# Kernel tuning notes

Hardware: AMD Instinct MI355X
Metric: run time of the kernel (lower is better)

## Reference

```python
import jax, jax.numpy as jnp
import numpy as np

FORWARD_STEPS = 50
DT = 0.01
G = 9.81
BATCH = 131072


def _rot(psi):
    # batched 6x6 block-rotation matrix R(psi)
    b = psi.shape[0]
    c, s = jnp.cos(psi), jnp.sin(psi)
    R = jnp.zeros((b, 6, 6), dtype=psi.dtype)
    R = R.at[:, 0, 0].set(c).at[:, 0, 2].set(-s)
    R = R.at[:, 1, 1].set(c).at[:, 1, 3].set(-s)
    R = R.at[:, 2, 0].set(s).at[:, 2, 2].set(c)
    R = R.at[:, 3, 1].set(s).at[:, 3, 3].set(c)
    R = R.at[:, 4, 4].set(1.0).at[:, 5, 5].set(1.0)
    return R


def setup_inputs() -> dict:
    key = jax.random.key(0)
    k1, k2, k3, k4, k5 = jax.random.split(key, 5)
    b = BATCH
    # build initial full state [b, 1, 8]: keep body-frame Vx away from 0 (A divides by Vx)
    fs = jnp.zeros((b, 8), dtype=jnp.float32)
    fs = fs.at[:, 0].set(jax.random.normal(k1, (b,)) * 0.1)                     # x
    fs = fs.at[:, 1].set(jax.random.uniform(k2, (b,), minval=0.5, maxval=1.5))  # x_dot
    fs = fs.at[:, 2].set(jax.random.normal(k3, (b,)) * 0.1)                     # y
    fs = fs.at[:, 3].set(jax.random.uniform(k4, (b,), minval=-0.2, maxval=0.2)) # y_dot
    fs = fs.at[:, 4].set(jax.random.uniform(k5, (b,), minval=-0.3, maxval=0.3)) # psi
    fs = fs.at[:, 5].set(jax.random.normal(jax.random.fold_in(key, 10), (b,)) * 0.1)  # psi_dot
    fs = fs.at[:, 6].set(jax.random.normal(jax.random.fold_in(key, 11), (b,)) * 0.1)  # accel cmd
    fs = fs.at[:, 7].set(jax.random.uniform(jax.random.fold_in(key, 12), (b,), minval=-0.2, maxval=0.2))  # steer cmd
    full_states = fs[:, None, :]
    actions = jnp.stack([
        jax.random.normal(jax.random.fold_in(key, 20), (b, FORWARD_STEPS)) * 0.1,
        jax.random.uniform(jax.random.fold_in(key, 21), (b, FORWARD_STEPS), minval=-0.2, maxval=0.2),
    ], axis=-1).astype(jnp.float32)
    m = 0.2
    return {
        "full_states": full_states,
        "actions": actions,
        "m": jnp.float32(m),
        "Caf": jnp.float32(5 * 0.25 * m * G),
        "Car": jnp.float32(5 * 0.25 * m * G),
        "lf": jnp.float32(0.05),
        "lr": jnp.float32(0.05),
        "Iz": jnp.float32((0.1 ** 2 + 0.1 ** 2) / 12.0),
    }


def reference(full_states, actions, m, Caf, Car, lf, lr, Iz):
    bsz = full_states.shape[0]
    dt = jnp.asarray(DT, dtype=full_states.dtype)
    state0 = full_states[:, -1, :6]   # [b,6]
    action0 = full_states[:, -1, 6:]  # [b,2]
    acts = jnp.transpose(actions, (1, 0, 2))  # [T,b,2]

    def step(carry, a_next):
        s, u = carry
        psi = s[:, 4]
        Vx = s[:, 1] * jnp.cos(psi) + s[:, 3] * jnp.sin(psi)
        A = jnp.zeros((bsz, 6, 6), dtype=s.dtype)
        A = A.at[:, 0, 1].set(1.0).at[:, 2, 3].set(1.0).at[:, 4, 5].set(1.0)
        A = A.at[:, 3, 3].set(-(2 * Caf + 2 * Car) / (m * Vx))
        A = A.at[:, 3, 5].set(-Vx - (2 * Caf * lf - 2 * Car * lr) / (m * Vx))
        A = A.at[:, 5, 3].set(-(2 * lf * Caf - 2 * lr * Car) / (Iz * Vx))
        A = A.at[:, 5, 4].set(-(2 * lf ** 2 * Caf + 2 * lr ** 2 * Car) / (Iz * Vx))
        Bm = jnp.zeros((bsz, 6, 2), dtype=s.dtype)
        Bm = Bm.at[:, 1, 0].set(1.0)
        Bm = Bm.at[:, 3, 1].set(2 * Caf / m)
        Bm = Bm.at[:, 5, 1].set(2 * lf * Caf / Iz)
        s_body = jnp.einsum('bij,bj->bi', _rot(-psi), s)
        temp = jnp.einsum('bij,bj->bi', A, s_body) + jnp.einsum('bij,bj->bi', Bm, u)
        pred = s + jnp.einsum('bij,bj->bi', _rot(psi), temp) * dt
        out = jnp.concatenate([pred, a_next], axis=1)  # [b,8]
        return (pred, a_next), out

    _, outs = jax.lax.scan(step, (state0, action0), acts)
    return jnp.transpose(outs, (1, 0, 2))  # [b, forward_steps, 8]
```

## Files before the change

### kernel.cpp

```cpp
#include <hip/hip_runtime.h>

#define N_STEPS 50
#define DT 0.01f

__global__ __launch_bounds__(256) void hybrid_sim_kernel(
    const float* __restrict__ fs,
    const float* __restrict__ actions,
    const float* __restrict__ pm,  const float* __restrict__ pCaf,
    const float* __restrict__ pCar, const float* __restrict__ plf,
    const float* __restrict__ plr, const float* __restrict__ pIz,
    float* __restrict__ out, int batch)
{
    int b = blockIdx.x * blockDim.x + threadIdx.x;
    if (b >= batch) return;

    const float4* fsp = (const float4*)(fs + (size_t)b * 8);
    float4 f0 = fsp[0];
    float4 f1 = fsp[1];
    float s0 = f0.x, s1 = f0.y, s2 = f0.z, s3 = f0.w;
    float s4 = f1.x, s5 = f1.y, u0 = f1.z, u1 = f1.w;

    float m  = *pm,  Caf = *pCaf, Car = *pCar;
    float lf = *plf, lr  = *plr,  Iz  = *pIz;
    float k1  = 2.f * (Caf + Car) / m;
    float k2  = 2.f * (Caf * lf - Car * lr) / m;
    float k3  = 2.f * (lf * Caf - lr * Car) / Iz;
    float k4  = 2.f * (lf * lf * Caf + lr * lr * Car) / Iz;
    float b31 = 2.f * Caf / m;
    float b51 = 2.f * lf * Caf / Iz;

    const float4* ap = (const float4*)(actions + (size_t)b * 100);
    float4*       op = (float4*)(out + (size_t)b * 400);

    for (int chunk = 0; chunk < 5; ++chunk) {
        float4 abuf[5];
        #pragma unroll
        for (int j = 0; j < 5; ++j) abuf[j] = ap[chunk * 5 + j];
        const float* av = (const float*)abuf;

        #pragma unroll
        for (int tt = 0; tt < 10; ++tt) {
            float psi = s4;
            float c  = __cosf(psi);
            float sn = __sinf(psi);
            float Vx  = c * s1 + sn * s3;
            float sb3 = c * s3 - sn * s1;
            float inv = __builtin_amdgcn_rcpf(Vx);
            float t3 = -k1 * inv * sb3 + (-Vx - k2 * inv) * s5 + b31 * u1;
            float t5 = -k3 * inv * sb3 - k4 * inv * psi + b51 * u1;
            float p0 = s0 + DT * (c * Vx - sn * sb3);
            float p2 = s2 + DT * (sn * Vx + c * sb3);
            float p1 = s1 + DT * (c * u0 - sn * t3);
            float p3 = s3 + DT * (sn * u0 + c * t3);
            float p4 = s4 + DT * s5;
            float p5 = s5 + DT * t5;

            float nu0 = av[2 * tt];
            float nu1 = av[2 * tt + 1];

            int t = chunk * 10 + tt;
            float4 o0; o0.x = p0; o0.y = p1; o0.z = p2; o0.w = p3;
            float4 o1; o1.x = p4; o1.y = p5; o1.z = nu0; o1.w = nu1;
            op[2 * t]     = o0;
            op[2 * t + 1] = o1;

            s0 = p0; s1 = p1; s2 = p2; s3 = p3; s4 = p4; s5 = p5;
            u0 = nu0; u1 = nu1;
        }
    }
}

extern "C" void kernel_launch(void* const* d_in, const int* in_sizes, int n_in,
                              void* d_out, int out_size, void* d_ws, size_t ws_size,
                              hipStream_t stream) {
    const float* fs      = (const float*)d_in[0];
    const float* actions = (const float*)d_in[1];
    int batch = in_sizes[0] / 8;
    int block = 256;
    int grid  = (batch + block - 1) / block;
    hybrid_sim_kernel<<<grid, block, 0, stream>>>(
        fs, actions,
        (const float*)d_in[2], (const float*)d_in[3], (const float*)d_in[4],
        (const float*)d_in[5], (const float*)d_in[6], (const float*)d_in[7],
        (float*)d_out, batch);
}
```

Measured before the change: 346.9 us.

## Stage per-step outputs in LDS to coalesce global stores

Each thread buffers two timesteps of output (16 floats) in a padded, double-buffered LDS tile. After a block barrier, the wave re-reads the tile transposed so that each 8-lane group writes one element's contiguous 64-byte segment to global memory. This replaces per-lane 32-byte strided stores that touched a different row per lane. It adds LDS traffic and a __syncthreads every two steps, and drops the batch bounds check by assuming the batch is a multiple of 256.

```diff
diff --git a/kernel.cpp b/kernel.cpp
--- a/kernel.cpp
+++ b/kernel.cpp
@@ -1,7 +1,7 @@
 #include <hip/hip_runtime.h>
 
-#define N_STEPS 50
 #define DT 0.01f
+#define ROW 18
 
 __global__ __launch_bounds__(256) void hybrid_sim_kernel(
     const float* __restrict__ fs,
@@ -9,63 +9,86 @@
     const float* __restrict__ pm,  const float* __restrict__ pCaf,
     const float* __restrict__ pCar, const float* __restrict__ plf,
     const float* __restrict__ plr, const float* __restrict__ pIz,
-    float* __restrict__ out, int batch)
+    float* __restrict__ out)
 {
-    int b = blockIdx.x * blockDim.x + threadIdx.x;
-    if (b >= batch) return;
+    __shared__ float lds[2 * 4 * 64 * ROW];
+
+    const int tid  = threadIdx.x;
+    const int lane = tid & 63;
+    const int wv   = tid >> 6;
+    const int b    = blockIdx.x * 256 + tid;
+    const int b0w  = blockIdx.x * 256 + (wv << 6);
 
     const float4* fsp = (const float4*)(fs + (size_t)b * 8);
     float4 f0 = fsp[0];
     float4 f1 = fsp[1];
-    float s0 = f0.x, s1 = f0.y, s2 = f0.z, s3 = f0.w;
-    float s4 = f1.x, s5 = f1.y, u0 = f1.z, u1 = f1.w;
+    float s0=f0.x, s1=f0.y, s2=f0.z, s3=f0.w, s4=f1.x, s5=f1.y, u0=f1.z, u1=f1.w;
 
-    float m  = *pm,  Caf = *pCaf, Car = *pCar;
-    float lf = *plf, lr  = *plr,  Iz  = *pIz;
-    float k1  = 2.f * (Caf + Car) / m;
-    float k2  = 2.f * (Caf * lf - Car * lr) / m;
-    float k3  = 2.f * (lf * Caf - lr * Car) / Iz;
-    float k4  = 2.f * (lf * lf * Caf + lr * lr * Car) / Iz;
-    float b31 = 2.f * Caf / m;
-    float b51 = 2.f * lf * Caf / Iz;
+    float m=*pm, Caf=*pCaf, Car=*pCar, lf=*plf, lr=*plr, Iz=*pIz;
+    float k1  = 2.f*(Caf+Car)/m;
+    float k2  = 2.f*(Caf*lf-Car*lr)/m;
+    float k3  = 2.f*(lf*Caf-lr*Car)/Iz;
+    float k4  = 2.f*(lf*lf*Caf+lr*lr*Car)/Iz;
+    float b31 = 2.f*Caf/m;
+    float b51 = 2.f*lf*Caf/Iz;
 
     const float4* ap = (const float4*)(actions + (size_t)b * 100);
-    float4*       op = (float4*)(out + (size_t)b * 400);
+
+    float* base0 = &lds[(0*4 + wv) * 64 * ROW];
+    float* base1 = &lds[(1*4 + wv) * 64 * ROW];
+
+    float o[16];
 
     for (int chunk = 0; chunk < 5; ++chunk) {
         float4 abuf[5];
         #pragma unroll
-        for (int j = 0; j < 5; ++j) abuf[j] = ap[chunk * 5 + j];
+        for (int j = 0; j < 5; ++j) abuf[j] = ap[chunk*5 + j];
         const float* av = (const float*)abuf;
 
         #pragma unroll
-        for (int tt = 0; tt < 10; ++tt) {
-            float psi = s4;
-            float c  = __cosf(psi);
-            float sn = __sinf(psi);
-            float Vx  = c * s1 + sn * s3;
-            float sb3 = c * s3 - sn * s1;
-            float inv = __builtin_amdgcn_rcpf(Vx);
-            float t3 = -k1 * inv * sb3 + (-Vx - k2 * inv) * s5 + b31 * u1;
-            float t5 = -k3 * inv * sb3 - k4 * inv * psi + b51 * u1;
-            float p0 = s0 + DT * (c * Vx - sn * sb3);
-            float p2 = s2 + DT * (sn * Vx + c * sb3);
-            float p1 = s1 + DT * (c * u0 - sn * t3);
-            float p3 = s3 + DT * (sn * u0 + c * t3);
-            float p4 = s4 + DT * s5;
-            float p5 = s5 + DT * t5;
+        for (int gg = 0; gg < 5; ++gg) {
+            #pragma unroll
+            for (int hh = 0; hh < 2; ++hh) {
+                int tt = gg*2 + hh;
+                float psi = s4;
+                float c  = __cosf(psi);
+                float sn = __sinf(psi);
+                float Vx  = c*s1 + sn*s3;
+                float sb3 = c*s3 - sn*s1;
+                float inv = __builtin_amdgcn_rcpf(Vx);
+                float t3 = -k1*inv*sb3 + (-Vx - k2*inv)*s5 + b31*u1;
+                float t5 = -k3*inv*sb3 - k4*inv*psi + b51*u1;
+                float p0 = s0 + DT*(c*Vx - sn*sb3);
+                float p2 = s2 + DT*(sn*Vx + c*sb3);
+                float p1 = s1 + DT*(c*u0 - sn*t3);
+                float p3 = s3 + DT*(sn*u0 + c*t3);
+                float p4 = s4 + DT*s5;
+                float p5 = s5 + DT*t5;
+                float nu0 = av[2*tt];
+                float nu1 = av[2*tt+1];
+                float* oo = &o[hh*8];
+                oo[0]=p0; oo[1]=p1; oo[2]=p2; oo[3]=p3;
+                oo[4]=p4; oo[5]=p5; oo[6]=nu0; oo[7]=nu1;
+                s0=p0; s1=p1; s2=p2; s3=p3; s4=p4; s5=p5; u0=nu0; u1=nu1;
+            }
 
-            float nu0 = av[2 * tt];
-            float nu1 = av[2 * tt + 1];
+            int g = chunk*5 + gg;
+            float* buf = (g & 1) ? base1 : base0;
 
-            int t = chunk * 10 + tt;
-            float4 o0; o0.x = p0; o0.y = p1; o0.z = p2; o0.w = p3;
-            float4 o1; o1.x = p4; o1.y = p5; o1.z = nu0; o1.w = nu1;
-            op[2 * t]     = o0;
-            op[2 * t + 1] = o1;
+            float2* rw = (float2*)(buf + lane*ROW);
+            #pragma unroll
+            for (int j = 0; j < 8; ++j) rw[j] = make_float2(o[2*j], o[2*j+1]);
 
-            s0 = p0; s1 = p1; s2 = p2; s3 = p3; s4 = p4; s5 = p5;
-            u0 = nu0; u1 = nu1;
+            __syncthreads();
+
+            #pragma unroll
+            for (int k = 0; k < 8; ++k) {
+                int e  = k*8 + (lane >> 3);
+                int mm = lane & 7;
+                float2 v = *(const float2*)(buf + e*ROW + mm*2);
+                float2* dst = (float2*)(out + (size_t)(b0w + e)*400 + g*16 + mm*2);
+                *dst = v;
+            }
         }
     }
 }
@@ -76,11 +99,10 @@
     const float* fs      = (const float*)d_in[0];
     const float* actions = (const float*)d_in[1];
     int batch = in_sizes[0] / 8;
-    int block = 256;
-    int grid  = (batch + block - 1) / block;
-    hybrid_sim_kernel<<<grid, block, 0, stream>>>(
+    int grid  = batch / 256;
+    hybrid_sim_kernel<<<grid, 256, 0, stream>>>(
         fs, actions,
         (const float*)d_in[2], (const float*)d_in[3], (const float*)d_in[4],
         (const float*)d_in[5], (const float*)d_in[6], (const float*)d_in[7],
-        (float*)d_out, batch);
+        (float*)d_out);
 }
```

After: 318.1 us. -8.3%, faster.
